# Kernel optimization log

Measured on AMD Instinct MI355X. Metric: run time of the kernel, lower is better.

Reference implementation:

```python
import jax, jax.numpy as jnp
import numpy as np

N_ATOMS, N_EDGES, N_TRIPLES = 5000, 200000, 4000000
D_NODE, D_EDGE, N_BASIS = 128, 128, 9


def setup_inputs() -> dict:
    key = jax.random.key(0)
    ks = jax.random.split(key, 14)
    inp = {
        "node_feat": jax.random.normal(ks[0], (N_ATOMS, D_NODE), jnp.float32),
        "edge_feat": jax.random.normal(ks[1], (N_EDGES, D_EDGE), jnp.float32),
        "three_basis": jax.random.normal(ks[2], (N_TRIPLES, N_BASIS), jnp.float32),
        "three_cutoff": jax.random.uniform(ks[3], (N_EDGES,), jnp.float32),
        # learned params: update_network_atom = Linear(d_node->n_basis) + sigmoid
        "W_atom": jax.random.normal(ks[4], (D_NODE, N_BASIS), jnp.float32) / np.sqrt(D_NODE).astype(np.float32),
        "b_atom": jnp.zeros((N_BASIS,), jnp.float32),
        # update_network_bond = gated MLP: silu(Linear) * sigmoid(Linear), n_basis->d_edge
        "W_gate": jax.random.normal(ks[5], (N_BASIS, D_EDGE), jnp.float32) / np.sqrt(N_BASIS).astype(np.float32),
        "b_gate": jnp.zeros((D_EDGE,), jnp.float32),
        "W_sig": jax.random.normal(ks[6], (N_BASIS, D_EDGE), jnp.float32) / np.sqrt(N_BASIS).astype(np.float32),
        "b_sig": jnp.zeros((D_EDGE,), jnp.float32),
        # graph structure (int constants)
        "graph_dst": jax.random.randint(ks[7], (N_EDGES,), 0, N_ATOMS, jnp.int32),
        "lg_src": jax.random.randint(ks[8], (N_TRIPLES,), 0, N_EDGES, jnp.int32),
        "lg_dst": jax.random.randint(ks[9], (N_TRIPLES,), 0, N_EDGES, jnp.int32),
        # sorted segment ids == get_segment_indices_from_n(n_triple_ij)
        "segment_ids": jnp.sort(jax.random.randint(ks[10], (N_TRIPLES,), 0, N_EDGES, jnp.int32)),
    }
    return inp


def reference(node_feat, edge_feat, three_basis, three_cutoff,
              W_atom, b_atom, W_gate, b_gate, W_sig, b_sig,
              graph_dst, lg_src, lg_dst, segment_ids):
    # Eq.2: transform node features, gather end atom of each triple's second bond
    atoms = jax.nn.sigmoid(node_feat @ W_atom + b_atom)          # [n_atoms, n_basis]
    end_atom_index = graph_dst[lg_dst]                           # [n_triples]
    basis = three_basis * atoms[end_atom_index]                  # [n_triples, n_basis]
    # cutoff weights per triple (dead code in the provided source: scatter uses basis)
    weights = three_cutoff[lg_src] * three_cutoff[lg_dst]        # [n_triples]
    _ = basis * weights[:, None]
    # scatter-sum triples back to their bond
    new_bonds = jax.ops.segment_sum(basis, segment_ids, num_segments=N_EDGES)  # [n_edges, n_basis]
    # Eq.3: gated MLP bond update
    update = jax.nn.silu(new_bonds @ W_gate + b_gate) * jax.nn.sigmoid(new_bonds @ W_sig + b_sig)
    return edge_feat + update
```

## Files before the change

### kernel.cpp

```cpp
#include <hip/hip_runtime.h>

#define D_NODE   128
#define N_BASIS  9
#define A_STRIDE 12
#define D_EDGE   128

#define BLOCK_C 256
#define TPT     4
#define CHUNK   (BLOCK_C * TPT)
#define SEG_CAP 512

__device__ __forceinline__ float fast_sigmoid(float x) {
    return __builtin_amdgcn_rcpf(1.0f + __expf(-x));
}

__global__ __launch_bounds__(256) void atoms_kernel(
    const float* __restrict__ node_feat,
    const float* __restrict__ W_atom,
    const float* __restrict__ b_atom,
    float* __restrict__ atoms, int n_atoms)
{
    __shared__ float sW[D_NODE * N_BASIS];
    for (int t = threadIdx.x; t < D_NODE * N_BASIS; t += 256)
        sW[t] = W_atom[t];
    __syncthreads();
    int idx = blockIdx.x * 256 + threadIdx.x;
    int total = n_atoms * N_BASIS;
    if (idx >= total) return;
    int a = idx / N_BASIS;
    int b = idx - a * N_BASIS;
    const float* row = node_feat + a * D_NODE;
    float acc = b_atom[b];
#pragma unroll 8
    for (int i = 0; i < D_NODE; ++i)
        acc += row[i] * sW[i * N_BASIS + b];
    atoms[a * A_STRIDE + b] = fast_sigmoid(acc);
}

#define FLUSH_RUN()                                                          \
    do {                                                                     \
        if (use_lds) {                                                       \
            float* dst_ = lacc + (cur - seg_first) * N_BASIS;                \
            _Pragma("unroll")                                                \
            for (int k_ = 0; k_ < N_BASIS; ++k_)                             \
                atomicAdd(&dst_[k_], sum[k_]);                               \
        } else {                                                             \
            float* dst_ = new_bonds + (size_t)cur * N_BASIS;                 \
            _Pragma("unroll")                                                \
            for (int k_ = 0; k_ < N_BASIS; ++k_)                             \
                unsafeAtomicAdd(&dst_[k_], sum[k_]);                         \
        }                                                                    \
    } while (0)

__global__ __launch_bounds__(BLOCK_C) void triple_kernel(
    const float* __restrict__ three_basis,
    const float* __restrict__ atoms,
    const int*   __restrict__ graph_dst,
    const int*   __restrict__ lg_dst,
    const int*   __restrict__ seg,
    float* __restrict__ new_bonds,
    int n_triples)
{
    __shared__ float lacc[SEG_CAP * N_BASIS];
    __shared__ int sh_first, sh_last;

    const int tid = threadIdx.x;
    const int chunk_start = blockIdx.x * CHUNK;
    const int t0 = chunk_start + tid * TPT;

    if (tid == 0) sh_first = seg[chunk_start];
    if (tid == BLOCK_C - 1) {
        int last = chunk_start + CHUNK;
        if (last > n_triples) last = n_triples;
        sh_last = seg[last - 1];
    }
    for (int i = tid; i < SEG_CAP * N_BASIS; i += BLOCK_C)
        lacc[i] = 0.0f;
    __syncthreads();

    const int seg_first = sh_first;
    const int range = sh_last - seg_first + 1;
    const bool use_lds = (range <= SEG_CAP);

    if (t0 + TPT <= n_triples) {
        float tb[TPT * N_BASIS];
        const float4* tb4 = (const float4*)(three_basis + (size_t)t0 * N_BASIS);
#pragma unroll
        for (int q = 0; q < 9; ++q)
            *(float4*)&tb[q * 4] = tb4[q];

        const int4 sg4 = *(const int4*)(seg + t0);
        const int4 ld4 = *(const int4*)(lg_dst + t0);
        int sgs[TPT]  = { sg4.x, sg4.y, sg4.z, sg4.w };
        int atomi[TPT];
        atomi[0] = graph_dst[ld4.x];
        atomi[1] = graph_dst[ld4.y];
        atomi[2] = graph_dst[ld4.z];
        atomi[3] = graph_dst[ld4.w];

        float sum[N_BASIS];
        int cur = sgs[0];
#pragma unroll
        for (int k = 0; k < N_BASIS; ++k) sum[k] = 0.0f;

#pragma unroll
        for (int i = 0; i < TPT; ++i) {
            if (sgs[i] != cur) {
                FLUSH_RUN();
                cur = sgs[i];
#pragma unroll
                for (int k = 0; k < N_BASIS; ++k) sum[k] = 0.0f;
            }
            const float4* ap = (const float4*)(atoms + (size_t)atomi[i] * A_STRIDE);
            float4 a0 = ap[0];
            float4 a1 = ap[1];
            float  a8 = ((const float*)ap)[8];
            sum[0] += tb[i * N_BASIS + 0] * a0.x;
            sum[1] += tb[i * N_BASIS + 1] * a0.y;
            sum[2] += tb[i * N_BASIS + 2] * a0.z;
            sum[3] += tb[i * N_BASIS + 3] * a0.w;
            sum[4] += tb[i * N_BASIS + 4] * a1.x;
            sum[5] += tb[i * N_BASIS + 5] * a1.y;
            sum[6] += tb[i * N_BASIS + 6] * a1.z;
            sum[7] += tb[i * N_BASIS + 7] * a1.w;
            sum[8] += tb[i * N_BASIS + 8] * a8;
        }
        FLUSH_RUN();
    } else if (t0 < n_triples) {
        for (int t = t0; t < n_triples; ++t) {
            int cur = seg[t];
            int atom = graph_dst[lg_dst[t]];
            const float* tbr = three_basis + (size_t)t * N_BASIS;
            const float* ar  = atoms + (size_t)atom * A_STRIDE;
            float sum[N_BASIS];
#pragma unroll
            for (int k = 0; k < N_BASIS; ++k) sum[k] = tbr[k] * ar[k];
            FLUSH_RUN();
        }
    }

    __syncthreads();

    if (use_lds) {
        int total = range * N_BASIS;
        for (int idx = tid; idx < total; idx += BLOCK_C) {
            int r = idx / N_BASIS;
            int k = idx - r * N_BASIS;
            float v = lacc[idx];
            int s = seg_first + r;
            if (r == 0 || r == range - 1) {
                if (v != 0.0f)
                    unsafeAtomicAdd(&new_bonds[(size_t)s * N_BASIS + k], v);
            } else {
                new_bonds[(size_t)s * N_BASIS + k] = v;
            }
        }
    }
}

__global__ __launch_bounds__(256) void mlp_kernel(
    const float* __restrict__ edge_feat,
    const float* __restrict__ new_bonds,
    const float* __restrict__ W_gate, const float* __restrict__ b_gate,
    const float* __restrict__ W_sig,  const float* __restrict__ b_sig,
    float* __restrict__ out, int n_edges)
{
    const int tid = threadIdx.x;
    const int grp = tid >> 5;
    const int c   = (tid & 31) * 4;
    const int e   = blockIdx.x * 8 + grp;
    if (e >= n_edges) return;

    float nb[N_BASIS];
    const float* nbr = new_bonds + (size_t)e * N_BASIS;
#pragma unroll
    for (int k = 0; k < N_BASIS; ++k) nb[k] = nbr[k];

    float4 g = *(const float4*)(b_gate + c);
    float4 s = *(const float4*)(b_sig + c);
#pragma unroll
    for (int k = 0; k < N_BASIS; ++k) {
        float4 wg = *(const float4*)(W_gate + k * D_EDGE + c);
        float4 ws = *(const float4*)(W_sig  + k * D_EDGE + c);
        g.x += nb[k] * wg.x; g.y += nb[k] * wg.y;
        g.z += nb[k] * wg.z; g.w += nb[k] * wg.w;
        s.x += nb[k] * ws.x; s.y += nb[k] * ws.y;
        s.z += nb[k] * ws.z; s.w += nb[k] * ws.w;
    }
    float4 ef = *(const float4*)(edge_feat + (size_t)e * D_EDGE + c);
    float4 o;
    o.x = ef.x + g.x * fast_sigmoid(g.x) * fast_sigmoid(s.x);
    o.y = ef.y + g.y * fast_sigmoid(g.y) * fast_sigmoid(s.y);
    o.z = ef.z + g.z * fast_sigmoid(g.z) * fast_sigmoid(s.z);
    o.w = ef.w + g.w * fast_sigmoid(g.w) * fast_sigmoid(s.w);
    *(float4*)(out + (size_t)e * D_EDGE + c) = o;
}

extern "C" void kernel_launch(void* const* d_in, const int* in_sizes, int n_in,
                              void* d_out, int out_size, void* d_ws, size_t ws_size,
                              hipStream_t stream) {
    const float* node_feat   = (const float*)d_in[0];
    const float* edge_feat   = (const float*)d_in[1];
    const float* three_basis = (const float*)d_in[2];
    const float* W_atom      = (const float*)d_in[4];
    const float* b_atom      = (const float*)d_in[5];
    const float* W_gate      = (const float*)d_in[6];
    const float* b_gate      = (const float*)d_in[7];
    const float* W_sig       = (const float*)d_in[8];
    const float* b_sig       = (const float*)d_in[9];
    const int*   graph_dst   = (const int*)d_in[10];
    const int*   lg_dst      = (const int*)d_in[12];
    const int*   seg         = (const int*)d_in[13];

    int n_atoms   = in_sizes[0] / D_NODE;
    int n_edges   = in_sizes[1] / D_EDGE;
    int n_triples = in_sizes[2] / N_BASIS;

    float* atoms = (float*)d_ws;
    size_t atoms_bytes = ((size_t)n_atoms * A_STRIDE * sizeof(float) + 255) & ~(size_t)255;
    float* new_bonds = (float*)((char*)d_ws + atoms_bytes);
    size_t nb_bytes = (size_t)n_edges * N_BASIS * sizeof(float);

    hipMemsetAsync(new_bonds, 0, nb_bytes, stream);

    atoms_kernel<<<(n_atoms * N_BASIS + 255) / 256, 256, 0, stream>>>(
        node_feat, W_atom, b_atom, atoms, n_atoms);

    triple_kernel<<<(n_triples + CHUNK - 1) / CHUNK, BLOCK_C, 0, stream>>>(
        three_basis, atoms, graph_dst, lg_dst, seg, new_bonds, n_triples);

    mlp_kernel<<<(n_edges + 7) / 8, 256, 0, stream>>>(
        edge_feat, new_bonds, W_gate, b_gate, W_sig, b_sig, (float*)d_out, n_edges);
}
```

Measured before the change: 462.7 us.

## Stage triple basis via LDS DMA, store atoms as fp16, batch MLP edges

```diff
diff --git a/kernel.cpp b/kernel.cpp
--- a/kernel.cpp
+++ b/kernel.cpp
@@ -1,14 +1,19 @@
 #include <hip/hip_runtime.h>
 
-#define D_NODE   128
-#define N_BASIS  9
-#define A_STRIDE 12
-#define D_EDGE   128
-
-#define BLOCK_C 256
-#define TPT     4
+#define D_NODE    128
+#define N_BASIS   9
+#define AH_STRIDE 16
+#define D_EDGE    128
+
+#define BLOCK_C 512
+#define TPT     2
 #define CHUNK   (BLOCK_C * TPT)
-#define SEG_CAP 512
+#define SEG_CAP 384
+
+typedef _Float16 half8 __attribute__((ext_vector_type(8)));
+
+#define AS1(p) ((const __attribute__((address_space(1))) void*)(p))
+#define AS3(p) ((__attribute__((address_space(3))) void*)(p))
 
 __device__ __forceinline__ float fast_sigmoid(float x) {
     return __builtin_amdgcn_rcpf(1.0f + __expf(-x));
@@ -18,7 +23,7 @@
     const float* __restrict__ node_feat,
     const float* __restrict__ W_atom,
     const float* __restrict__ b_atom,
-    float* __restrict__ atoms, int n_atoms)
+    _Float16* __restrict__ atoms, int n_atoms)
 {
     __shared__ float sW[D_NODE * N_BASIS];
     for (int t = threadIdx.x; t < D_NODE * N_BASIS; t += 256)
@@ -34,7 +39,7 @@
 #pragma unroll 8
     for (int i = 0; i < D_NODE; ++i)
         acc += row[i] * sW[i * N_BASIS + b];
-    atoms[a * A_STRIDE + b] = fast_sigmoid(acc);
+    atoms[a * AH_STRIDE + b] = (_Float16)fast_sigmoid(acc);
 }
 
 #define FLUSH_RUN()                                                          \
@@ -54,19 +59,40 @@
 
 __global__ __launch_bounds__(BLOCK_C) void triple_kernel(
     const float* __restrict__ three_basis,
-    const float* __restrict__ atoms,
+    const _Float16* __restrict__ atoms,
     const int*   __restrict__ graph_dst,
     const int*   __restrict__ lg_dst,
     const int*   __restrict__ seg,
     float* __restrict__ new_bonds,
     int n_triples)
 {
+    __shared__ float stb[CHUNK * N_BASIS];
     __shared__ float lacc[SEG_CAP * N_BASIS];
     __shared__ int sh_first, sh_last;
 
     const int tid = threadIdx.x;
     const int chunk_start = blockIdx.x * CHUNK;
     const int t0 = chunk_start + tid * TPT;
+
+    {
+        int avail = (n_triples - chunk_start) * (N_BASIS * 4);
+        int full_bytes = avail > CHUNK * N_BASIS * 4 ? CHUNK * N_BASIS * 4 : avail;
+        int nfull = full_bytes >> 4;
+        const char* gsrc = (const char*)three_basis + (size_t)chunk_start * (N_BASIS * 4);
+        const int lane = tid & 63;
+        for (int base = (tid >> 6) * 64; base < nfull; base += BLOCK_C) {
+            int i = base + lane;
+            if (i < nfull) {
+                __builtin_amdgcn_global_load_lds(
+                    AS1(gsrc + (size_t)i * 16),
+                    AS3((char*)stb + (size_t)base * 16),
+                    16, 0, 0);
+            }
+        }
+        int rem = full_bytes - (nfull << 4);
+        if ((tid << 2) < rem)
+            ((float*)stb)[nfull * 4 + tid] = ((const float*)gsrc)[nfull * 4 + tid];
+    }
 
     if (tid == 0) sh_first = seg[chunk_start];
     if (tid == BLOCK_C - 1) {
@@ -76,65 +102,60 @@
     }
     for (int i = tid; i < SEG_CAP * N_BASIS; i += BLOCK_C)
         lacc[i] = 0.0f;
+
+    const bool fast = (t0 + TPT <= n_triples);
+    int sg0 = 0, sg1 = 0;
+    half8 h0, h1;
+    _Float16 e0h = (_Float16)0.f, e1h = (_Float16)0.f;
+    if (fast) {
+        int2 sg2 = *(const int2*)(seg + t0);
+        int2 ld2 = *(const int2*)(lg_dst + t0);
+        sg0 = sg2.x; sg1 = sg2.y;
+        int ai0 = graph_dst[ld2.x];
+        int ai1 = graph_dst[ld2.y];
+        const _Float16* ap0 = atoms + (size_t)ai0 * AH_STRIDE;
+        const _Float16* ap1 = atoms + (size_t)ai1 * AH_STRIDE;
+        h0 = *(const half8*)ap0;
+        h1 = *(const half8*)ap1;
+        e0h = ap0[8];
+        e1h = ap1[8];
+    }
+
     __syncthreads();
 
     const int seg_first = sh_first;
     const int range = sh_last - seg_first + 1;
     const bool use_lds = (range <= SEG_CAP);
 
-    if (t0 + TPT <= n_triples) {
-        float tb[TPT * N_BASIS];
-        const float4* tb4 = (const float4*)(three_basis + (size_t)t0 * N_BASIS);
-#pragma unroll
-        for (int q = 0; q < 9; ++q)
-            *(float4*)&tb[q * 4] = tb4[q];
-
-        const int4 sg4 = *(const int4*)(seg + t0);
-        const int4 ld4 = *(const int4*)(lg_dst + t0);
-        int sgs[TPT]  = { sg4.x, sg4.y, sg4.z, sg4.w };
-        int atomi[TPT];
-        atomi[0] = graph_dst[ld4.x];
-        atomi[1] = graph_dst[ld4.y];
-        atomi[2] = graph_dst[ld4.z];
-        atomi[3] = graph_dst[ld4.w];
-
+    if (fast) {
+        const float* tbl = stb + tid * (TPT * N_BASIS);
         float sum[N_BASIS];
-        int cur = sgs[0];
-#pragma unroll
-        for (int k = 0; k < N_BASIS; ++k) sum[k] = 0.0f;
-
-#pragma unroll
-        for (int i = 0; i < TPT; ++i) {
-            if (sgs[i] != cur) {
-                FLUSH_RUN();
-                cur = sgs[i];
-#pragma unroll
-                for (int k = 0; k < N_BASIS; ++k) sum[k] = 0.0f;
-            }
-            const float4* ap = (const float4*)(atoms + (size_t)atomi[i] * A_STRIDE);
-            float4 a0 = ap[0];
-            float4 a1 = ap[1];
-            float  a8 = ((const float*)ap)[8];
-            sum[0] += tb[i * N_BASIS + 0] * a0.x;
-            sum[1] += tb[i * N_BASIS + 1] * a0.y;
-            sum[2] += tb[i * N_BASIS + 2] * a0.z;
-            sum[3] += tb[i * N_BASIS + 3] * a0.w;
-            sum[4] += tb[i * N_BASIS + 4] * a1.x;
-            sum[5] += tb[i * N_BASIS + 5] * a1.y;
-            sum[6] += tb[i * N_BASIS + 6] * a1.z;
-            sum[7] += tb[i * N_BASIS + 7] * a1.w;
-            sum[8] += tb[i * N_BASIS + 8] * a8;
+        int cur = sg0;
+#pragma unroll
+        for (int k = 0; k < 8; ++k) sum[k] = tbl[k] * (float)h0[k];
+        sum[8] = tbl[8] * (float)e0h;
+        if (sg1 != cur) {
+            FLUSH_RUN();
+            cur = sg1;
+#pragma unroll
+            for (int k = 0; k < 8; ++k) sum[k] = tbl[N_BASIS + k] * (float)h1[k];
+            sum[8] = tbl[N_BASIS + 8] * (float)e1h;
+        } else {
+#pragma unroll
+            for (int k = 0; k < 8; ++k) sum[k] += tbl[N_BASIS + k] * (float)h1[k];
+            sum[8] += tbl[N_BASIS + 8] * (float)e1h;
         }
         FLUSH_RUN();
     } else if (t0 < n_triples) {
-        for (int t = t0; t < n_triples; ++t) {
+        int tend = t0 + TPT; if (tend > n_triples) tend = n_triples;
+        for (int t = t0; t < tend; ++t) {
             int cur = seg[t];
             int atom = graph_dst[lg_dst[t]];
             const float* tbr = three_basis + (size_t)t * N_BASIS;
-            const float* ar  = atoms + (size_t)atom * A_STRIDE;
+            const _Float16* ar = atoms + (size_t)atom * AH_STRIDE;
             float sum[N_BASIS];
 #pragma unroll
-            for (int k = 0; k < N_BASIS; ++k) sum[k] = tbr[k] * ar[k];
+            for (int k = 0; k < N_BASIS; ++k) sum[k] = tbr[k] * (float)ar[k];
             FLUSH_RUN();
         }
     }
@@ -165,35 +186,53 @@
     const float* __restrict__ W_sig,  const float* __restrict__ b_sig,
     float* __restrict__ out, int n_edges)
 {
-    const int tid = threadIdx.x;
-    const int grp = tid >> 5;
-    const int c   = (tid & 31) * 4;
-    const int e   = blockIdx.x * 8 + grp;
-    if (e >= n_edges) return;
-
-    float nb[N_BASIS];
-    const float* nbr = new_bonds + (size_t)e * N_BASIS;
-#pragma unroll
-    for (int k = 0; k < N_BASIS; ++k) nb[k] = nbr[k];
-
-    float4 g = *(const float4*)(b_gate + c);
-    float4 s = *(const float4*)(b_sig + c);
+    const int tid  = threadIdx.x;
+    const int grp  = tid >> 5;
+    const int c    = (tid & 31) * 4;
+    const int e0   = (blockIdx.x * 8 + grp) * 4;
+    if (e0 >= n_edges) return;
+    const int nvalid = (n_edges - e0) < 4 ? (n_edges - e0) : 4;
+
+    float nb[4][N_BASIS];
+#pragma unroll
+    for (int j = 0; j < 4; ++j) {
+        const float* nbr = new_bonds + (size_t)(e0 + (j < nvalid ? j : 0)) * N_BASIS;
+#pragma unroll
+        for (int k = 0; k < N_BASIS; ++k) nb[j][k] = nbr[k];
+    }
+
+    float4 bg = *(const float4*)(b_gate + c);
+    float4 bs = *(const float4*)(b_sig + c);
+    float4 g[4], s[4];
+#pragma unroll
+    for (int j = 0; j < 4; ++j) { g[j] = bg; s[j] = bs; }
+
 #pragma unroll
     for (int k = 0; k < N_BASIS; ++k) {
         float4 wg = *(const float4*)(W_gate + k * D_EDGE + c);
         float4 ws = *(const float4*)(W_sig  + k * D_EDGE + c);
-        g.x += nb[k] * wg.x; g.y += nb[k] * wg.y;
-        g.z += nb[k] * wg.z; g.w += nb[k] * wg.w;
-        s.x += nb[k] * ws.x; s.y += nb[k] * ws.y;
-        s.z += nb[k] * ws.z; s.w += nb[k] * ws.w;
-    }
-    float4 ef = *(const float4*)(edge_feat + (size_t)e * D_EDGE + c);
-    float4 o;
-    o.x = ef.x + g.x * fast_sigmoid(g.x) * fast_sigmoid(s.x);
-    o.y = ef.y + g.y * fast_sigmoid(g.y) * fast_sigmoid(s.y);
-    o.z = ef.z + g.z * fast_sigmoid(g.z) * fast_sigmoid(s.z);
-    o.w = ef.w + g.w * fast_sigmoid(g.w) * fast_sigmoid(s.w);
-    *(float4*)(out + (size_t)e * D_EDGE + c) = o;
+#pragma unroll
+        for (int j = 0; j < 4; ++j) {
+            g[j].x += nb[j][k] * wg.x; g[j].y += nb[j][k] * wg.y;
+            g[j].z += nb[j][k] * wg.z; g[j].w += nb[j][k] * wg.w;
+            s[j].x += nb[j][k] * ws.x; s[j].y += nb[j][k] * ws.y;
+            s[j].z += nb[j][k] * ws.z; s[j].w += nb[j][k] * ws.w;
+        }
+    }
+
+#pragma unroll
+    for (int j = 0; j < 4; ++j) {
+        if (j < nvalid) {
+            int e = e0 + j;
+            float4 ef = *(const float4*)(edge_feat + (size_t)e * D_EDGE + c);
+            float4 o;
+            o.x = ef.x + g[j].x * fast_sigmoid(g[j].x) * fast_sigmoid(s[j].x);
+            o.y = ef.y + g[j].y * fast_sigmoid(g[j].y) * fast_sigmoid(s[j].y);
+            o.z = ef.z + g[j].z * fast_sigmoid(g[j].z) * fast_sigmoid(s[j].z);
+            o.w = ef.w + g[j].w * fast_sigmoid(g[j].w) * fast_sigmoid(s[j].w);
+            *(float4*)(out + (size_t)e * D_EDGE + c) = o;
+        }
+    }
 }
 
 extern "C" void kernel_launch(void* const* d_in, const int* in_sizes, int n_in,
@@ -216,8 +255,8 @@
     int n_edges   = in_sizes[1] / D_EDGE;
     int n_triples = in_sizes[2] / N_BASIS;
 
-    float* atoms = (float*)d_ws;
-    size_t atoms_bytes = ((size_t)n_atoms * A_STRIDE * sizeof(float) + 255) & ~(size_t)255;
+    _Float16* atoms = (_Float16*)d_ws;
+    size_t atoms_bytes = ((size_t)n_atoms * AH_STRIDE * sizeof(_Float16) + 255) & ~(size_t)255;
     float* new_bonds = (float*)((char*)d_ws + atoms_bytes);
     size_t nb_bytes = (size_t)n_edges * N_BASIS * sizeof(float);
 
@@ -229,6 +268,6 @@
     triple_kernel<<<(n_triples + CHUNK - 1) / CHUNK, BLOCK_C, 0, stream>>>(
         three_basis, atoms, graph_dst, lg_dst, seg, new_bonds, n_triples);
 
-    mlp_kernel<<<(n_edges + 7) / 8, 256, 0, stream>>>(
+    mlp_kernel<<<(n_edges + 31) / 32, 256, 0, stream>>>(
         edge_feat, new_bonds, W_gate, b_gate, W_sig, b_sig, (float*)d_out, n_edges);
 }
```

After: 474.8 us. 1.03x slower.
